# Kernel tuning notes

Hardware: AMD Instinct MI355X
Metric: run time of the kernel (lower is better)

Reference implementation:

```python
import jax, jax.numpy as jnp
import numpy as np

N, D, E, R, G, M = 8192, 1024, 64, 64, 8, 8

def setup_inputs() -> dict:
    key = jax.random.key(0)
    k_h, k_wg, k_wl, k_w1, k_w2 = jax.random.split(key, 5)
    return {
        'h': jax.random.normal(k_h, (N, D), jnp.float32),
        'Wg': jax.random.normal(k_wg, (D, G), jnp.float32) * 0.02,  # nn.Linear weight (transposed)
        'bg': jnp.zeros((G,), jnp.float32),
        'Wloc': jax.random.normal(k_wl, (G, D, M), jnp.float32) * 0.02,
        'W1': jax.random.normal(k_w1, (E, D, R), jnp.float32) * 0.02,
        'W2': jax.random.normal(k_w2, (E, R, D), jnp.float32) * 0.02,
        'k': 2,
    }

def reference(h, Wg, bg, Wloc, W1, W2, k):
    n, d = h.shape
    g, _, m = Wloc.shape
    e = W1.shape[0]
    router_temp = 1.0
    # stage 1: group routing (top-1)
    g_scores = h @ Wg + bg                                   # (N, G)
    group_idx = jnp.argmax(g_scores, axis=-1)                # (N,)
    # stage 2: within-group scores; compute all groups (cheap: N*G*M) then select
    all_local = jnp.einsum('nd,gdm->ngm', h, Wloc)           # (N, G, M)
    local_scores = jnp.take_along_axis(all_local, group_idx[:, None, None], axis=1)[:, 0]  # (N, M)
    topv, topm = jax.lax.top_k(local_scores, k)              # (N, k)
    gate = jax.nn.softmax(topv / max(router_temp, 1e-6), axis=-1)
    expert_ids = group_idx[:, None] * m + topm               # (N, k) global expert ids
    # scatter gates into dense (N, E); topm entries are distinct per token
    gate_full = jnp.zeros((n, e), h.dtype).at[jnp.arange(n)[:, None], expert_ids].set(gate)
    # low-rank expert compute: relu(h @ W1) @ W2, weighted-combined
    tmp = jax.nn.relu(jnp.einsum('nd,edr->ner', h, W1))      # (N, E, R)
    out = jnp.einsum('ner,erd->nd', gate_full[:, :, None] * tmp, W2)  # (N, D)
    return out, expert_ids, gate, group_idx
```

## Files before the change

kernel.cpp:

```cpp
#include <hip/hip_runtime.h>
#include <hip/hip_bf16.h>
#include <cstdint>
#include <cstddef>

#define NTOK 8192
#define DIM  1024
#define NEXP 64
#define RANK 64
#define NGRP 8
#define NLOC 8

typedef __attribute__((ext_vector_type(8))) short bf16x8;
typedef __attribute__((ext_vector_type(4))) float f32x4;

static __device__ inline unsigned int pack_bf16x2(float a, float b) {
    __hip_bfloat16 ha = __float2bfloat16(a);
    __hip_bfloat16 hb = __float2bfloat16(b);
    return (unsigned int)(*(unsigned short*)&ha) |
           ((unsigned int)(*(unsigned short*)&hb) << 16);
}

__global__ __launch_bounds__(256, 2) void score_kernel(
    const float* __restrict__ h, const float* __restrict__ Wg,
    const float* __restrict__ Wloc, float* __restrict__ S_cm)
{
    __shared__ float Hs[32][65];
    __shared__ float Bs[64][80];

    const int t0 = blockIdx.x * 32;
    const int tx = threadIdx.x & 15;
    const int ty = threadIdx.x >> 4;

    float acc[2][4] = {};
    float accs[2] = {};

    for (int kc = 0; kc < DIM; kc += 64) {
        __syncthreads();
#pragma unroll
        for (int it = 0; it < 8; ++it) {
            const int idx = threadIdx.x + it * 256;
            const int r = idx >> 6, c = idx & 63;
            Hs[r][c] = h[(size_t)(t0 + r) * DIM + kc + c];
        }
#pragma unroll 8
        for (int it = 0; it < 16; ++it) {
            const int idx = threadIdx.x + it * 256;
            const int k = idx >> 6, c = idx & 63;
            Bs[k][c] = Wloc[(size_t)(c >> 3) * (DIM * NLOC) + (size_t)(kc + k) * NLOC + (c & 7)];
        }
#pragma unroll
        for (int it = 0; it < 2; ++it) {
            const int idx = threadIdx.x + it * 256;
            const int k = idx >> 3, c8 = idx & 7;
            Bs[k][64 + c8] = Wg[(size_t)(kc + k) * NGRP + c8];
            Bs[k][72 + c8] = 0.f;
        }
        __syncthreads();
#pragma unroll 8
        for (int k = 0; k < 64; ++k) {
            const float a0 = Hs[tx][k];
            const float a1 = Hs[tx + 16][k];
            const float4 b = *(const float4*)&Bs[k][ty * 4];
            const float bs = Bs[k][64 + ty];
            acc[0][0] += a0 * b.x; acc[0][1] += a0 * b.y;
            acc[0][2] += a0 * b.z; acc[0][3] += a0 * b.w;
            acc[1][0] += a1 * b.x; acc[1][1] += a1 * b.y;
            acc[1][2] += a1 * b.z; acc[1][3] += a1 * b.w;
            accs[0] += a0 * bs;
            accs[1] += a1 * bs;
        }
    }
#pragma unroll
    for (int i = 0; i < 2; ++i) {
        const int t = t0 + tx + 16 * i;
#pragma unroll
        for (int j = 0; j < 4; ++j)
            S_cm[(size_t)(ty * 4 + j) * NTOK + t] = acc[i][j];
        if (ty < 8)
            S_cm[(size_t)(64 + ty) * NTOK + t] = accs[i];
    }
}

__global__ __launch_bounds__(256) void route_kernel(
    const float* __restrict__ S_cm, const float* __restrict__ bg,
    float* __restrict__ out_eid, float* __restrict__ out_gate,
    float* __restrict__ out_gidx,
    int* __restrict__ ws_eids, float* __restrict__ ws_gates,
    int* __restrict__ counts)
{
    __shared__ int hist[NEXP];
    if (threadIdx.x < NEXP) hist[threadIdx.x] = 0;
    __syncthreads();

    const int t = blockIdx.x * 256 + threadIdx.x;

    float best = S_cm[(size_t)64 * NTOK + t] + bg[0];
    int gi = 0;
#pragma unroll
    for (int g = 1; g < NGRP; ++g) {
        const float v = S_cm[(size_t)(64 + g) * NTOK + t] + bg[g];
        if (v > best) { best = v; gi = g; }
    }
    float ls[NLOC];
#pragma unroll
    for (int m = 0; m < NLOC; ++m) ls[m] = S_cm[(size_t)(gi * NLOC + m) * NTOK + t];
    int m1 = 0; float v1 = ls[0];
#pragma unroll
    for (int m = 1; m < NLOC; ++m) { if (ls[m] > v1) { v1 = ls[m]; m1 = m; } }
    int m2 = (m1 == 0) ? 1 : 0; float v2 = ls[m2];
#pragma unroll
    for (int m = 0; m < NLOC; ++m) {
        if (m != m1 && m != ((m1 == 0) ? 1 : 0) && ls[m] > v2) { v2 = ls[m]; m2 = m; }
    }
    const float e2v = expf(v2 - v1);
    const float inv = 1.f / (1.f + e2v);
    const float g0 = inv, g1 = e2v * inv;
    const int e0 = gi * NLOC + m1, e1 = gi * NLOC + m2;

    out_eid[t * 2 + 0] = (float)e0;
    out_eid[t * 2 + 1] = (float)e1;
    out_gate[t * 2 + 0] = g0;
    out_gate[t * 2 + 1] = g1;
    out_gidx[t] = (float)gi;
    ws_eids[t * 2 + 0] = e0;
    ws_eids[t * 2 + 1] = e1;
    ws_gates[t * 2 + 0] = g0;
    ws_gates[t * 2 + 1] = g1;
    atomicAdd(&hist[e0], 1);
    atomicAdd(&hist[e1], 1);

    __syncthreads();
    if (threadIdx.x < NEXP) atomicAdd(&counts[threadIdx.x], hist[threadIdx.x]);
}

__global__ __launch_bounds__(64) void scan_kernel(
    const int* __restrict__ counts, int* __restrict__ offsets, int* __restrict__ cursor)
{
    const int e = threadIdx.x;
    const int c = counts[e];
    int s = c;
#pragma unroll
    for (int d = 1; d < 64; d <<= 1) {
        int v = __shfl_up(s, d, 64);
        if (e >= d) s += v;
    }
    offsets[e] = s - c;
    cursor[e] = s - c;
    if (e == 63) offsets[64] = s;
}

__global__ __launch_bounds__(256) void scatter_kernel(
    const int* __restrict__ ws_eids, const float* __restrict__ ws_gates,
    int* __restrict__ cursor, int* __restrict__ token_list, float* __restrict__ slot_gate)
{
    const int t = blockIdx.x * 256 + threadIdx.x;
    if (t >= NTOK) return;
#pragma unroll
    for (int j = 0; j < 2; ++j) {
        const int eid = ws_eids[t * 2 + j];
        const int pos = atomicAdd(&cursor[eid], 1);
        token_list[pos] = t * 2 + j;
        slot_gate[pos] = ws_gates[t * 2 + j];
    }
}

__global__ __launch_bounds__(256) void cast_h(
    const float* __restrict__ h, unsigned short* __restrict__ hb)
{
    const size_t i0 = ((size_t)blockIdx.x * 256 + threadIdx.x) * 8;
    const float4 x = *(const float4*)(h + i0);
    const float4 y = *(const float4*)(h + i0 + 4);
    uint4 v;
    v.x = pack_bf16x2(x.x, x.y);
    v.y = pack_bf16x2(x.z, x.w);
    v.z = pack_bf16x2(y.x, y.y);
    v.w = pack_bf16x2(y.z, y.w);
    *(uint4*)(hb + i0) = v;
}

__global__ __launch_bounds__(256) void prep_w1(
    const float* __restrict__ W1, unsigned short* __restrict__ W1t)
{
    __shared__ float Ls[64][65];
    const int e = blockIdx.x, kb = blockIdx.y;
    const float* src = W1 + (size_t)e * DIM * RANK + (size_t)kb * 64 * RANK;
#pragma unroll
    for (int it = 0; it < 4; ++it) {
        const int kk = (threadIdx.x >> 4) + it * 16;
        const int rr = (threadIdx.x & 15) * 4;
        *(float4*)&Ls[kk][rr] = *(const float4*)(src + (size_t)kk * RANK + rr);
    }
    __syncthreads();
#pragma unroll
    for (int it = 0; it < 2; ++it) {
        const int idx = threadIdx.x + it * 256;
        const int r = idx >> 3, k8 = (idx & 7) * 8;
        uint4 v;
        v.x = pack_bf16x2(Ls[k8 + 0][r], Ls[k8 + 1][r]);
        v.y = pack_bf16x2(Ls[k8 + 2][r], Ls[k8 + 3][r]);
        v.z = pack_bf16x2(Ls[k8 + 4][r], Ls[k8 + 5][r]);
        v.w = pack_bf16x2(Ls[k8 + 6][r], Ls[k8 + 7][r]);
        *(uint4*)(W1t + (size_t)e * RANK * DIM + (size_t)r * DIM + kb * 64 + k8) = v;
    }
}

__global__ __launch_bounds__(256) void prep_w2(
    const float* __restrict__ W2, unsigned short* __restrict__ W2t)
{
    __shared__ float Ls[64][65];
    const int e = blockIdx.x, db = blockIdx.y;
    const float* src = W2 + (size_t)e * RANK * DIM + db * 64;
#pragma unroll
    for (int it = 0; it < 4; ++it) {
        const int rr = (threadIdx.x >> 4) + it * 16;
        const int dd = (threadIdx.x & 15) * 4;
        *(float4*)&Ls[rr][dd] = *(const float4*)(src + (size_t)rr * DIM + dd);
    }
    __syncthreads();
#pragma unroll
    for (int it = 0; it < 2; ++it) {
        const int idx = threadIdx.x + it * 256;
        const int d = idx >> 3, r8 = (idx & 7) * 8;
        uint4 v;
        v.x = pack_bf16x2(Ls[r8 + 0][d], Ls[r8 + 1][d]);
        v.y = pack_bf16x2(Ls[r8 + 2][d], Ls[r8 + 3][d]);
        v.z = pack_bf16x2(Ls[r8 + 4][d], Ls[r8 + 5][d]);
        v.w = pack_bf16x2(Ls[r8 + 6][d], Ls[r8 + 7][d]);
        *(uint4*)(W2t + (size_t)e * DIM * RANK + (size_t)(db * 64 + d) * RANK + r8) = v;
    }
}

__global__ __launch_bounds__(256, 2) void e1_mfma(
    const unsigned short* __restrict__ hb, const unsigned short* __restrict__ W1t,
    const int* __restrict__ offsets, const int* __restrict__ token_list,
    const float* __restrict__ slot_gate, unsigned short* __restrict__ P)
{
    __shared__ unsigned short Hs[64 * 72];
    __shared__ unsigned short Ws[64 * 72];
    __shared__ int   tokS[64];
    __shared__ float gateS[64];

    const int e  = blockIdx.x;
    const int n0 = offsets[e];
    const int ne = offsets[e + 1] - n0;
    const unsigned short* W1te = W1t + (size_t)e * RANK * DIM;
    const int tid  = threadIdx.x;
    const int wave = tid >> 6;
    const int lane = tid & 63;
    const int tx   = lane & 15;
    const int quad = lane >> 4;

    for (int tile = blockIdx.y; tile * 64 < ne; tile += 8) {
        const int row0 = tile * 64;
        __syncthreads();
        if (tid < 64) {
            const int gr = row0 + tid;
            tokS[tid]  = (gr < ne) ? token_list[n0 + gr] : -1;
            gateS[tid] = (gr < ne) ? slot_gate[n0 + gr] : 0.f;
        }
        f32x4 acc[4] = {};
        for (int kc = 0; kc < DIM; kc += 64) {
            __syncthreads();
#pragma unroll
            for (int it = 0; it < 2; ++it) {
                const int idx = tid + it * 256;
                const int s = idx >> 3, k8 = (idx & 7) * 8;
                const int ent = tokS[s];
                uint4 v = make_uint4(0, 0, 0, 0);
                if (ent >= 0)
                    v = *(const uint4*)(hb + (size_t)(ent >> 1) * DIM + kc + k8);
                *(uint4*)(Hs + s * 72 + k8) = v;
            }
#pragma unroll
            for (int it = 0; it < 2; ++it) {
                const int idx = tid + it * 256;
                const int r = idx >> 3, k8 = (idx & 7) * 8;
                *(uint4*)(Ws + r * 72 + k8) =
                    *(const uint4*)(W1te + (size_t)r * DIM + kc + k8);
            }
            __syncthreads();
#pragma unroll
            for (int ks = 0; ks < 2; ++ks) {
                const bf16x8 a = *(const bf16x8*)(Hs + (wave * 16 + tx) * 72 + ks * 32 + quad * 8);
#pragma unroll
                for (int j = 0; j < 4; ++j) {
                    const bf16x8 b = *(const bf16x8*)(Ws + (j * 16 + tx) * 72 + ks * 32 + quad * 8);
                    acc[j] = __builtin_amdgcn_mfma_f32_16x16x32_bf16(a, b, acc[j], 0, 0, 0);
                }
            }
        }
#pragma unroll
        for (int j = 0; j < 4; ++j) {
#pragma unroll
            for (int i = 0; i < 4; ++i) {
                const int sl = wave * 16 + quad * 4 + i;
                const int gr = row0 + sl;
                if (gr < ne) {
                    const float v = fmaxf(acc[j][i], 0.f) * gateS[sl];
                    __hip_bfloat16 hv = __float2bfloat16(v);
                    P[(size_t)(n0 + gr) * RANK + j * 16 + tx] = *(unsigned short*)&hv;
                }
            }
        }
    }
}

__global__ __launch_bounds__(256, 2) void e2_mfma(
    const unsigned short* __restrict__ P, const unsigned short* __restrict__ W2t,
    const int* __restrict__ offsets, const int* __restrict__ token_list,
    float* __restrict__ out, float* __restrict__ contrib)
{
    __shared__ unsigned short Ps[64 * 72];
    __shared__ unsigned short W2s[64 * 72];
    __shared__ int tokS[64];

    const int e = blockIdx.x;
    const int colbase = blockIdx.y * 64;
    const int n0 = offsets[e];
    const int ne = offsets[e + 1] - n0;
    const unsigned short* W2te = W2t + (size_t)e * DIM * RANK;
    const int tid  = threadIdx.x;
    const int wave = tid >> 6;
    const int lane = tid & 63;
    const int tx   = lane & 15;
    const int quad = lane >> 4;

#pragma unroll
    for (int it = 0; it < 2; ++it) {
        const int idx = tid + it * 256;
        const int d = idx >> 3, r8 = (idx & 7) * 8;
        *(uint4*)(W2s + d * 72 + r8) =
            *(const uint4*)(W2te + (size_t)(colbase + d) * RANK + r8);
    }

    for (int tile = blockIdx.z; tile * 64 < ne; tile += 4) {
        const int row0 = tile * 64;
        __syncthreads();
        if (tid < 64) {
            const int gr = row0 + tid;
            tokS[tid] = (gr < ne) ? token_list[n0 + gr] : -1;
        }
#pragma unroll
        for (int it = 0; it < 2; ++it) {
            const int idx = tid + it * 256;
            const int s = idx >> 3, r8 = (idx & 7) * 8;
            const int gr = row0 + s;
            uint4 v = make_uint4(0, 0, 0, 0);
            if (gr < ne) v = *(const uint4*)(P + (size_t)(n0 + gr) * RANK + r8);
            *(uint4*)(Ps + s * 72 + r8) = v;
        }
        __syncthreads();
        f32x4 acc[4] = {};
#pragma unroll
        for (int ks = 0; ks < 2; ++ks) {
            const bf16x8 a = *(const bf16x8*)(Ps + (wave * 16 + tx) * 72 + ks * 32 + quad * 8);
#pragma unroll
            for (int j = 0; j < 4; ++j) {
                const bf16x8 b = *(const bf16x8*)(W2s + (j * 16 + tx) * 72 + ks * 32 + quad * 8);
                acc[j] = __builtin_amdgcn_mfma_f32_16x16x32_bf16(a, b, acc[j], 0, 0, 0);
            }
        }
#pragma unroll
        for (int i = 0; i < 4; ++i) {
            const int sl = wave * 16 + quad * 4 + i;
            const int ent = tokS[sl];
            if (ent >= 0) {
                float* base = (ent & 1) ? contrib : out;
                float* op = base + (size_t)(ent >> 1) * DIM + colbase;
#pragma unroll
                for (int j = 0; j < 4; ++j)
                    op[j * 16 + tx] = acc[j][i];
            }
        }
    }
}

__global__ __launch_bounds__(256) void combine_kernel(
    const float* __restrict__ contrib, float* __restrict__ out)
{
    const size_t i = (size_t)blockIdx.x * 256 + threadIdx.x;
    float4 a = ((const float4*)out)[i];
    const float4 b = ((const float4*)contrib)[i];
    a.x += b.x; a.y += b.y; a.z += b.z; a.w += b.w;
    ((float4*)out)[i] = a;
}

extern "C" void kernel_launch(void* const* d_in, const int* in_sizes, int n_in,
                              void* d_out, int out_size, void* d_ws, size_t ws_size,
                              hipStream_t stream)
{
    const float* h    = (const float*)d_in[0];
    const float* Wg   = (const float*)d_in[1];
    const float* bg   = (const float*)d_in[2];
    const float* Wloc = (const float*)d_in[3];
    const float* W1   = (const float*)d_in[4];
    const float* W2   = (const float*)d_in[5];

    float* out_f    = (float*)d_out;
    float* out_main = out_f;
    float* out_eid  = out_f + (size_t)NTOK * DIM;
    float* out_gate = out_eid + (size_t)NTOK * 2;
    float* out_gidx = out_gate + (size_t)NTOK * 2;

    int* ws_i        = (int*)d_ws;
    int* counts      = ws_i;
    int* offsets     = ws_i + 64;
    int* cursor      = ws_i + 192;
    int* ws_eids     = ws_i + 256;
    int* token_list  = ws_i + 256 + 16384;
    float* ws_f      = (float*)(ws_i + 256 + 2 * 16384);
    float* ws_gates  = ws_f;
    float* slot_gate = ws_f + 16384;
    unsigned short* P_h  = (unsigned short*)(ws_f + 2 * 16384);
    unsigned short* W1t  = P_h + (size_t)16384 * RANK;
    unsigned short* W2t  = W1t + (size_t)NEXP * RANK * DIM;
    float* contrib       = (float*)(W2t + (size_t)NEXP * DIM * RANK);
    float* S_cm = contrib;
    unsigned short* hb = (unsigned short*)contrib;

    hipMemsetAsync(counts, 0, 64 * sizeof(int), stream);

    prep_w1<<<dim3(NEXP, 16), 256, 0, stream>>>(W1, W1t);
    prep_w2<<<dim3(NEXP, 16), 256, 0, stream>>>(W2, W2t);
    score_kernel<<<NTOK / 32, 256, 0, stream>>>(h, Wg, Wloc, S_cm);
    route_kernel<<<NTOK / 256, 256, 0, stream>>>(S_cm, bg,
        out_eid, out_gate, out_gidx, ws_eids, ws_gates, counts);
    scan_kernel<<<1, 64, 0, stream>>>(counts, offsets, cursor);
    scatter_kernel<<<NTOK / 256, 256, 0, stream>>>(ws_eids, ws_gates, cursor,
        token_list, slot_gate);
    cast_h<<<(NTOK * DIM / 8) / 256, 256, 0, stream>>>(h, hb);
    e1_mfma<<<dim3(NEXP, 8), 256, 0, stream>>>(hb, W1t, offsets, token_list,
        slot_gate, P_h);
    e2_mfma<<<dim3(NEXP, 16, 4), 256, 0, stream>>>(P_h, W2t, offsets, token_list,
        out_main, contrib);
    combine_kernel<<<(NTOK * DIM / 4) / 256, 256, 0, stream>>>(contrib, out_main);
}
```

Before: 273.3 us.

## Split routing into group-score pass and grouped local-score pass; fuse bf16 cast

The old single pass computed all 64 within-group local scores plus 8 group scores for every token. The new code first computes only the group scores and argmax, writing bf16 h as a side effect so the separate cast kernel goes away. It then buckets tokens by group and computes only the 8 local scores of the chosen group for each token. This removes most of the local-score FLOPs, but adds a scatter kernel and a second read of h with gathered rows, and the per-group workload can be imbalanced.

```diff
diff --git a/kernel.cpp b/kernel.cpp
--- a/kernel.cpp
+++ b/kernel.cpp
@@ -20,90 +20,180 @@
            ((unsigned int)(*(unsigned short*)&hb) << 16);
 }
 
-__global__ __launch_bounds__(256, 2) void score_kernel(
+__global__ __launch_bounds__(256, 4) void score_g_cast(
     const float* __restrict__ h, const float* __restrict__ Wg,
-    const float* __restrict__ Wloc, float* __restrict__ S_cm)
-{
-    __shared__ float Hs[32][65];
-    __shared__ float Bs[64][80];
-
-    const int t0 = blockIdx.x * 32;
-    const int tx = threadIdx.x & 15;
-    const int ty = threadIdx.x >> 4;
-
-    float acc[2][4] = {};
-    float accs[2] = {};
-
+    const float* __restrict__ bg, unsigned short* __restrict__ hb,
+    float* __restrict__ out_gidx, int* __restrict__ gidx_i,
+    int* __restrict__ counts_g)
+{
+    __shared__ float Hs[16][66];
+    __shared__ float Bs[64 * 8];
+    __shared__ float Sp[16][16][8];
+    __shared__ float Sg[16][9];
+    __shared__ int   hist_g[NGRP];
+
+    const int t0  = blockIdx.x * 16;
+    const int tid = threadIdx.x;
+    const int t   = tid & 15;
+    const int kq  = tid >> 4;
+    const int kbase = (kq >> 2) * 16 + (kq & 3);
+
+    if (tid < NGRP) hist_g[tid] = 0;
+
+    float acc[8] = {};
     for (int kc = 0; kc < DIM; kc += 64) {
         __syncthreads();
-#pragma unroll
-        for (int it = 0; it < 8; ++it) {
-            const int idx = threadIdx.x + it * 256;
-            const int r = idx >> 6, c = idx & 63;
-            Hs[r][c] = h[(size_t)(t0 + r) * DIM + kc + c];
-        }
-#pragma unroll 8
-        for (int it = 0; it < 16; ++it) {
-            const int idx = threadIdx.x + it * 256;
-            const int k = idx >> 6, c = idx & 63;
-            Bs[k][c] = Wloc[(size_t)(c >> 3) * (DIM * NLOC) + (size_t)(kc + k) * NLOC + (c & 7)];
-        }
-#pragma unroll
-        for (int it = 0; it < 2; ++it) {
-            const int idx = threadIdx.x + it * 256;
-            const int k = idx >> 3, c8 = idx & 7;
-            Bs[k][64 + c8] = Wg[(size_t)(kc + k) * NGRP + c8];
-            Bs[k][72 + c8] = 0.f;
-        }
-        __syncthreads();
-#pragma unroll 8
-        for (int k = 0; k < 64; ++k) {
-            const float a0 = Hs[tx][k];
-            const float a1 = Hs[tx + 16][k];
-            const float4 b = *(const float4*)&Bs[k][ty * 4];
-            const float bs = Bs[k][64 + ty];
-            acc[0][0] += a0 * b.x; acc[0][1] += a0 * b.y;
-            acc[0][2] += a0 * b.z; acc[0][3] += a0 * b.w;
-            acc[1][0] += a1 * b.x; acc[1][1] += a1 * b.y;
-            acc[1][2] += a1 * b.z; acc[1][3] += a1 * b.w;
-            accs[0] += a0 * bs;
-            accs[1] += a1 * bs;
-        }
-    }
-#pragma unroll
-    for (int i = 0; i < 2; ++i) {
-        const int t = t0 + tx + 16 * i;
-#pragma unroll
-        for (int j = 0; j < 4; ++j)
-            S_cm[(size_t)(ty * 4 + j) * NTOK + t] = acc[i][j];
-        if (ty < 8)
-            S_cm[(size_t)(64 + ty) * NTOK + t] = accs[i];
-    }
-}
-
-__global__ __launch_bounds__(256) void route_kernel(
-    const float* __restrict__ S_cm, const float* __restrict__ bg,
+        {
+            const int r = tid >> 4, c4 = tid & 15;
+            const float4 v = *(const float4*)(h + (size_t)(t0 + r) * DIM + kc + c4 * 4);
+            *(float2*)&Hs[r][c4 * 4]     = make_float2(v.x, v.y);
+            *(float2*)&Hs[r][c4 * 4 + 2] = make_float2(v.z, v.w);
+            uint2 pk;
+            pk.x = pack_bf16x2(v.x, v.y);
+            pk.y = pack_bf16x2(v.z, v.w);
+            *(uint2*)(hb + (size_t)(t0 + r) * DIM + kc + c4 * 4) = pk;
+        }
+        {
+            const float* src = Wg + (size_t)kc * NGRP;
+            Bs[tid] = src[tid];
+            Bs[tid + 256] = src[tid + 256];
+        }
+        __syncthreads();
+#pragma unroll
+        for (int kk = 0; kk < 4; ++kk) {
+            const int k = kbase + kk * 4;
+            const float a = Hs[t][k];
+            const float4 b0 = *(const float4*)&Bs[k * 8];
+            const float4 b1 = *(const float4*)&Bs[k * 8 + 4];
+            acc[0] += a * b0.x; acc[1] += a * b0.y; acc[2] += a * b0.z; acc[3] += a * b0.w;
+            acc[4] += a * b1.x; acc[5] += a * b1.y; acc[6] += a * b1.z; acc[7] += a * b1.w;
+        }
+    }
+#pragma unroll
+    for (int m = 0; m < 8; ++m) Sp[t][kq][m] = acc[m];
+    __syncthreads();
+    if (tid < 128) {
+        const int tt = tid >> 3, m = tid & 7;
+        float s = 0.f;
+#pragma unroll
+        for (int q = 0; q < 16; ++q) s += Sp[tt][q][m];
+        Sg[tt][m] = s + bg[m];
+    }
+    __syncthreads();
+    if (tid < 16) {
+        int gi = 0; float best = Sg[tid][0];
+#pragma unroll
+        for (int g = 1; g < NGRP; ++g) {
+            if (Sg[tid][g] > best) { best = Sg[tid][g]; gi = g; }
+        }
+        out_gidx[t0 + tid] = (float)gi;
+        gidx_i[t0 + tid] = gi;
+        atomicAdd(&hist_g[gi], 1);
+    }
+    __syncthreads();
+    if (tid < NGRP) atomicAdd(&counts_g[tid], hist_g[tid]);
+}
+
+__global__ __launch_bounds__(256) void scatter_g(
+    const int* __restrict__ gidx_i, const int* __restrict__ counts_g,
+    int* __restrict__ cursor_g, int* __restrict__ glist)
+{
+    const int t = blockIdx.x * 256 + threadIdx.x;
+    const int g = gidx_i[t];
+    int base = 0;
+    for (int gg = 0; gg < g; ++gg) base += counts_g[gg];
+    const int pos = base + atomicAdd(&cursor_g[g], 1);
+    glist[pos] = t;
+}
+
+__global__ __launch_bounds__(256, 4) void score_loc(
+    const float* __restrict__ h, const float* __restrict__ Wloc,
+    const int* __restrict__ counts_g, const int* __restrict__ glist,
+    float* __restrict__ S_loc)
+{
+    __shared__ float Hs[16][66];
+    __shared__ float Bs[64 * 8];
+    __shared__ float Sp[16][16][8];
+    __shared__ int   tokS[16];
+
+    const int g = blockIdx.x;
+    int base = 0;
+    for (int gg = 0; gg < g; ++gg) base += counts_g[gg];
+    const int ng = counts_g[g];
+    const float* Wl = Wloc + (size_t)g * DIM * NLOC;
+    const int tid = threadIdx.x;
+    const int t   = tid & 15;
+    const int kq  = tid >> 4;
+    const int kbase = (kq >> 2) * 16 + (kq & 3);
+
+    for (int tile = blockIdx.y; tile * 16 < ng; tile += gridDim.y) {
+        __syncthreads();
+        if (tid < 16) {
+            const int gr = tile * 16 + tid;
+            tokS[tid] = (gr < ng) ? glist[base + gr] : -1;
+        }
+        float acc[8] = {};
+        for (int kc = 0; kc < DIM; kc += 64) {
+            __syncthreads();
+            {
+                const int r = tid >> 4, c4 = tid & 15;
+                const int tok = tokS[r];
+                float4 v = make_float4(0.f, 0.f, 0.f, 0.f);
+                if (tok >= 0)
+                    v = *(const float4*)(h + (size_t)tok * DIM + kc + c4 * 4);
+                *(float2*)&Hs[r][c4 * 4]     = make_float2(v.x, v.y);
+                *(float2*)&Hs[r][c4 * 4 + 2] = make_float2(v.z, v.w);
+            }
+            {
+                const float* src = Wl + (size_t)kc * NLOC;
+                Bs[tid] = src[tid];
+                Bs[tid + 256] = src[tid + 256];
+            }
+            __syncthreads();
+#pragma unroll
+            for (int kk = 0; kk < 4; ++kk) {
+                const int k = kbase + kk * 4;
+                const float a = Hs[t][k];
+                const float4 b0 = *(const float4*)&Bs[k * 8];
+                const float4 b1 = *(const float4*)&Bs[k * 8 + 4];
+                acc[0] += a * b0.x; acc[1] += a * b0.y; acc[2] += a * b0.z; acc[3] += a * b0.w;
+                acc[4] += a * b1.x; acc[5] += a * b1.y; acc[6] += a * b1.z; acc[7] += a * b1.w;
+            }
+        }
+#pragma unroll
+        for (int m = 0; m < 8; ++m) Sp[t][kq][m] = acc[m];
+        __syncthreads();
+        if (tid < 128) {
+            const int tt = tid >> 3, m = tid & 7;
+            const int tok = tokS[tt];
+            if (tok >= 0) {
+                float s = 0.f;
+#pragma unroll
+                for (int q = 0; q < 16; ++q) s += Sp[tt][q][m];
+                S_loc[(size_t)tok * NLOC + m] = s;
+            }
+        }
+    }
+}
+
+__global__ __launch_bounds__(256) void route2(
+    const float* __restrict__ S_loc, const int* __restrict__ gidx_i,
     float* __restrict__ out_eid, float* __restrict__ out_gate,
-    float* __restrict__ out_gidx,
     int* __restrict__ ws_eids, float* __restrict__ ws_gates,
-    int* __restrict__ counts)
+    int* __restrict__ counts_e)
 {
     __shared__ int hist[NEXP];
     if (threadIdx.x < NEXP) hist[threadIdx.x] = 0;
     __syncthreads();
 
     const int t = blockIdx.x * 256 + threadIdx.x;
-
-    float best = S_cm[(size_t)64 * NTOK + t] + bg[0];
-    int gi = 0;
-#pragma unroll
-    for (int g = 1; g < NGRP; ++g) {
-        const float v = S_cm[(size_t)(64 + g) * NTOK + t] + bg[g];
-        if (v > best) { best = v; gi = g; }
-    }
+    const int gi = gidx_i[t];
     float ls[NLOC];
-#pragma unroll
-    for (int m = 0; m < NLOC; ++m) ls[m] = S_cm[(size_t)(gi * NLOC + m) * NTOK + t];
+    const float4 l0 = *(const float4*)(S_loc + (size_t)t * NLOC);
+    const float4 l1 = *(const float4*)(S_loc + (size_t)t * NLOC + 4);
+    ls[0] = l0.x; ls[1] = l0.y; ls[2] = l0.z; ls[3] = l0.w;
+    ls[4] = l1.x; ls[5] = l1.y; ls[6] = l1.z; ls[7] = l1.w;
+
     int m1 = 0; float v1 = ls[0];
 #pragma unroll
     for (int m = 1; m < NLOC; ++m) { if (ls[m] > v1) { v1 = ls[m]; m1 = m; } }
@@ -121,7 +211,6 @@
     out_eid[t * 2 + 1] = (float)e1;
     out_gate[t * 2 + 0] = g0;
     out_gate[t * 2 + 1] = g1;
-    out_gidx[t] = (float)gi;
     ws_eids[t * 2 + 0] = e0;
     ws_eids[t * 2 + 1] = e1;
     ws_gates[t * 2 + 0] = g0;
@@ -130,7 +219,7 @@
     atomicAdd(&hist[e1], 1);
 
     __syncthreads();
-    if (threadIdx.x < NEXP) atomicAdd(&counts[threadIdx.x], hist[threadIdx.x]);
+    if (threadIdx.x < NEXP) atomicAdd(&counts_e[threadIdx.x], hist[threadIdx.x]);
 }
 
 __global__ __launch_bounds__(64) void scan_kernel(
@@ -149,7 +238,7 @@
     if (e == 63) offsets[64] = s;
 }
 
-__global__ __launch_bounds__(256) void scatter_kernel(
+__global__ __launch_bounds__(256) void scatter_e(
     const int* __restrict__ ws_eids, const float* __restrict__ ws_gates,
     int* __restrict__ cursor, int* __restrict__ token_list, float* __restrict__ slot_gate)
 {
@@ -162,20 +251,6 @@
         token_list[pos] = t * 2 + j;
         slot_gate[pos] = ws_gates[t * 2 + j];
     }
-}
-
-__global__ __launch_bounds__(256) void cast_h(
-    const float* __restrict__ h, unsigned short* __restrict__ hb)
-{
-    const size_t i0 = ((size_t)blockIdx.x * 256 + threadIdx.x) * 8;
-    const float4 x = *(const float4*)(h + i0);
-    const float4 y = *(const float4*)(h + i0 + 4);
-    uint4 v;
-    v.x = pack_bf16x2(x.x, x.y);
-    v.y = pack_bf16x2(x.z, x.w);
-    v.z = pack_bf16x2(y.x, y.y);
-    v.w = pack_bf16x2(y.z, y.w);
-    *(uint4*)(hb + i0) = v;
 }
 
 __global__ __launch_bounds__(256) void prep_w1(
@@ -403,35 +478,41 @@
     float* out_gidx = out_gate + (size_t)NTOK * 2;
 
     int* ws_i        = (int*)d_ws;
-    int* counts      = ws_i;
-    int* offsets     = ws_i + 64;
-    int* cursor      = ws_i + 192;
-    int* ws_eids     = ws_i + 256;
-    int* token_list  = ws_i + 256 + 16384;
-    float* ws_f      = (float*)(ws_i + 256 + 2 * 16384);
+    int* counts_e    = ws_i;
+    int* offsets_e   = ws_i + 64;
+    int* cursor_e    = ws_i + 192;
+    int* counts_g    = ws_i + 256;
+    int* cursor_g    = ws_i + 264;
+    int* gidx_i      = ws_i + 512;
+    int* glist       = ws_i + 8704;
+    int* ws_eids     = ws_i + 16896;
+    int* token_list  = ws_i + 33280;
+    float* ws_f      = (float*)(ws_i + 49664);
     float* ws_gates  = ws_f;
     float* slot_gate = ws_f + 16384;
-    unsigned short* P_h  = (unsigned short*)(ws_f + 2 * 16384);
-    unsigned short* W1t  = P_h + (size_t)16384 * RANK;
-    unsigned short* W2t  = W1t + (size_t)NEXP * RANK * DIM;
-    float* contrib       = (float*)(W2t + (size_t)NEXP * DIM * RANK);
-    float* S_cm = contrib;
+    float* S_loc     = ws_f + 2 * 16384;
+    unsigned short* P_h = (unsigned short*)(ws_f + 2 * 16384 + 65536);
+    unsigned short* W1t = P_h + (size_t)16384 * RANK;
+    unsigned short* W2t = W1t + (size_t)NEXP * RANK * DIM;
+    float* contrib      = (float*)(W2t + (size_t)NEXP * DIM * RANK);
     unsigned short* hb = (unsigned short*)contrib;
 
-    hipMemsetAsync(counts, 0, 64 * sizeof(int), stream);
+    hipMemsetAsync(ws_i, 0, 272 * sizeof(int), stream);
 
     prep_w1<<<dim3(NEXP, 16), 256, 0, stream>>>(W1, W1t);
     prep_w2<<<dim3(NEXP, 16), 256, 0, stream>>>(W2, W2t);
-    score_kernel<<<NTOK / 32, 256, 0, stream>>>(h, Wg, Wloc, S_cm);
-    route_kernel<<<NTOK / 256, 256, 0, stream>>>(S_cm, bg,
-        out_eid, out_gate, out_gidx, ws_eids, ws_gates, counts);
-    scan_kernel<<<1, 64, 0, stream>>>(counts, offsets, cursor);
-    scatter_kernel<<<NTOK / 256, 256, 0, stream>>>(ws_eids, ws_gates, cursor,
+    score_g_cast<<<NTOK / 16, 256, 0, stream>>>(h, Wg, bg, hb,
+        out_gidx, gidx_i, counts_g);
+    scatter_g<<<NTOK / 256, 256, 0, stream>>>(gidx_i, counts_g, cursor_g, glist);
+    score_loc<<<dim3(NGRP, 64), 256, 0, stream>>>(h, Wloc, counts_g, glist, S_loc);
+    route2<<<NTOK / 256, 256, 0, stream>>>(S_loc, gidx_i,
+        out_eid, out_gate, ws_eids, ws_gates, counts_e);
+    scan_kernel<<<1, 64, 0, stream>>>(counts_e, offsets_e, cursor_e);
+    scatter_e<<<NTOK / 256, 256, 0, stream>>>(ws_eids, ws_gates, cursor_e,
         token_list, slot_gate);
-    cast_h<<<(NTOK * DIM / 8) / 256, 256, 0, stream>>>(h, hb);
-    e1_mfma<<<dim3(NEXP, 8), 256, 0, stream>>>(hb, W1t, offsets, token_list,
+    e1_mfma<<<dim3(NEXP, 8), 256, 0, stream>>>(hb, W1t, offsets_e, token_list,
         slot_gate, P_h);
-    e2_mfma<<<dim3(NEXP, 16, 4), 256, 0, stream>>>(P_h, W2t, offsets, token_list,
+    e2_mfma<<<dim3(NEXP, 16, 4), 256, 0, stream>>>(P_h, W2t, offsets_e, token_list,
         out_main, contrib);
     combine_kernel<<<(NTOK * DIM / 4) / 256, 256, 0, stream>>>(contrib, out_main);
 }
```

Measured after the change: 272.8 us. No clear change (-0.2%).
